# Kernel tuning notes

Hardware: AMD Instinct MI355X
Metric: run time of the kernel (lower is better)

## Reference

```python
import jax, jax.numpy as jnp
import numpy as np


def setup_inputs() -> dict:
    key = jax.random.key(0)
    k1, k2, k3 = jax.random.split(key, 3)
    m, n, d = 4096, 8192, 128
    sub_graph = jax.random.uniform(k1, (m, n), dtype=jnp.float32)
    sub_x = jax.random.normal(k2, (m, d), dtype=jnp.float32)
    all_x = jax.random.normal(k3, (n, d), dtype=jnp.float32)
    return {"sub_graph": sub_graph, "sub_x": sub_x, "all_x": all_x}


def reference(sub_graph, sub_x, all_x):
    # graph_loss, 2D branch. Algebraically identical to the torch code:
    #   trace(X^T diag(d) X) = sum_i d_i * ||x_i||^2
    #   trace(A^T G B)       = sum(A * (G @ B))
    # This avoids materializing the [m,m]/[n,n] diag matrices.
    row_deg = sub_graph.sum(axis=1)            # [m]
    col_deg = sub_graph.sum(axis=0)            # [n]
    term0 = jnp.sum(row_deg * jnp.sum(sub_x * sub_x, axis=1))
    term1 = jnp.sum(col_deg * jnp.sum(all_x * all_x, axis=1))
    cross = jnp.sum(sub_x * (sub_graph @ all_x))
    loss = term0 + term1 - 2.0 * cross
    m, n = sub_graph.shape
    return loss / (m * n)
```

## Files before the change

### kernel.cpp

```cpp
#include <hip/hip_runtime.h>
#include <hip/hip_bf16.h>

#define M 4096
#define N 8192
#define D 128

typedef __attribute__((ext_vector_type(8))) short short8_t;
typedef __attribute__((ext_vector_type(16))) float f32x16;

__device__ inline unsigned short f2bf(float f) {
    union { float f; unsigned u; } v; v.f = f;
    unsigned r = v.u + 0x7FFFu + ((v.u >> 16) & 1u);
    return (unsigned short)(r >> 16);
}


__global__ __launch_bounds__(256) void prep_kernel(const float* __restrict__ sub_x,
                                                   const float* __restrict__ all_x,
                                                   float* __restrict__ ws,
                                                   float* __restrict__ out) {
    const int wave = threadIdx.x >> 6;
    const int lane = threadIdx.x & 63;
    const int row  = blockIdx.x * 4 + wave;

    unsigned* sxb = (unsigned*)(ws + M + N);
    unsigned* axb = sxb + (size_t)M * 64;

    const float* src; float* ndst; unsigned* tdst; int r, R;
    if (row < M) { r = row;     src = sub_x + (size_t)r * D; ndst = ws + r;     tdst = sxb; R = M; }
    else         { r = row - M; src = all_x + (size_t)r * D; ndst = ws + M + r; tdst = axb; R = N; }

    const float2 v = ((const float2*)src)[lane];

    float s = v.x * v.x + v.y * v.y;
    #pragma unroll
    for (int off = 32; off > 0; off >>= 1) s += __shfl_down(s, off, 64);
    if (lane == 0) ndst[0] = s;

    const unsigned p = ((unsigned)f2bf(v.y) << 16) | (unsigned)f2bf(v.x);
    const int k8 = lane >> 2, q = lane & 3;
    tdst[((size_t)k8 * R + r) * 4 + q] = p;

    if (blockIdx.x == 0 && threadIdx.x == 0) out[0] = 0.0f;
}

__global__ __launch_bounds__(256, 3) void graph_loss_kernel(const float* __restrict__ G,
                                                            const float* __restrict__ ws,
                                                            float* __restrict__ out) {
    __shared__ float red[4];

    const int tid  = threadIdx.x;
    const int lane = tid & 63;
    const int w    = tid >> 6;
    const int c    = lane & 31;
    const int hw   = lane >> 5;

    const int ti = blockIdx.x >> 6;
    const int tj = blockIdx.x & 63;
    const int i0 = ti * 128;
    const int j0 = tj * 128;

    const float* sxn = ws;
    const float* axn = ws + M;
    const uint4* sxb = (const uint4*)(ws + M + N);
    const uint4* axb = sxb + (size_t)16 * M;

    const float* gbase = G + (size_t)(i0 + w * 32 + 4 * hw) * N + j0 + c;

    float gv[2][16];
    #pragma unroll
    for (int r = 0; r < 16; ++r)
        gv[0][r] = gbase[(size_t)((r & 3) + 8 * (r >> 2)) * N];

    short8_t a_frag[8];
    #pragma unroll
    for (int kk = 0; kk < 8; ++kk) {
        const uint4 t = sxb[(size_t)(kk * 2 + hw) * M + i0 + w * 32 + c];
        a_frag[kk] = *(const short8_t*)&t;
    }

    float sxv[16];
    #pragma unroll
    for (int r = 0; r < 16; ++r)
        sxv[r] = sxn[i0 + w * 32 + (r & 3) + 8 * (r >> 2) + 4 * hw];

    float axv[4];
    #pragma unroll
    for (int jt = 0; jt < 4; ++jt)
        axv[jt] = axn[j0 + jt * 32 + c];

    const uint4* bbase = axb + (size_t)hw * N + j0 + c;

    float local = 0.0f;

    #pragma unroll
    for (int jt = 0; jt < 4; ++jt) {
        if (jt < 3) {
            #pragma unroll
            for (int r = 0; r < 16; ++r)
                gv[(jt + 1) & 1][r] = gbase[(size_t)((r & 3) + 8 * (r >> 2)) * N + (jt + 1) * 32];
        }

        short8_t b[8];
        #pragma unroll
        for (int kk = 0; kk < 8; ++kk) {
            const uint4 t = bbase[(size_t)(kk * 2) * N + jt * 32];
            b[kk] = *(const short8_t*)&t;
        }

        f32x16 acc;
        #pragma unroll
        for (int r = 0; r < 16; ++r) acc[r] = 0.0f;

        #pragma unroll
        for (int kk = 0; kk < 8; ++kk)
            acc = __builtin_amdgcn_mfma_f32_32x32x16_bf16(a_frag[kk], b[kk], acc, 0, 0, 0);

        const float av = axv[jt];
        #pragma unroll
        for (int r = 0; r < 16; ++r)
            local += gv[jt & 1][r] * (sxv[r] + av - 2.0f * acc[r]);
    }

    #pragma unroll
    for (int off = 32; off > 0; off >>= 1) local += __shfl_down(local, off, 64);
    if (lane == 0) red[w] = local;
    __syncthreads();
    if (tid == 0) {
        const float bsum = red[0] + red[1] + red[2] + red[3];
        atomicAdd(out, bsum * (1.0f / 33554432.0f));
    }
}

extern "C" void kernel_launch(void* const* d_in, const int* in_sizes, int n_in,
                              void* d_out, int out_size, void* d_ws, size_t ws_size,
                              hipStream_t stream) {
    const float* G      = (const float*)d_in[0];
    const float* sub_x  = (const float*)d_in[1];
    const float* all_x  = (const float*)d_in[2];
    float* out = (float*)d_out;
    float* ws  = (float*)d_ws;

    prep_kernel<<<(M + N) / 4, 256, 0, stream>>>(sub_x, all_x, ws, out);
    graph_loss_kernel<<<(M / 128) * (N / 128), 256, 0, stream>>>(G, ws, out);
}
```

Measured before the change: 200.2 us.

## Retile to 32x1024 strips with LDS-staged MFMA results and float4 G loads

Changes the block tile from 128x128 to 32 rows by 1024 columns. Each wave computes the 32x32 MFMA tile for its own column chunk and writes the combined weights (row norm + column norm - 2*dot) into a double-buffered LDS array. G is then read as coalesced float4 rows and multiplied against those weights from LDS. The goal is wide, streaming reads of G with software prefetch two chunks ahead, and reuse of the a-fragment across 1024 columns. The cost is a barrier per chunk and extra LDS traffic.

```diff
diff --git a/kernel.cpp b/kernel.cpp
--- a/kernel.cpp
+++ b/kernel.cpp
@@ -4,6 +4,11 @@
 #define M 4096
 #define N 8192
 #define D 128
+
+#define I_T 32
+#define J_T 1024
+#define JC  128
+#define NC  (J_T / JC)
 
 typedef __attribute__((ext_vector_type(8))) short short8_t;
 typedef __attribute__((ext_vector_type(16))) float f32x16;
@@ -13,7 +18,6 @@
     unsigned r = v.u + 0x7FFFu + ((v.u >> 16) & 1u);
     return (unsigned short)(r >> 16);
 }
-
 
 __global__ __launch_bounds__(256) void prep_kernel(const float* __restrict__ sub_x,
                                                    const float* __restrict__ all_x,
@@ -44,9 +48,47 @@
     if (blockIdx.x == 0 && threadIdx.x == 0) out[0] = 0.0f;
 }
 
+#define PHASE(T, GC, PBASE, QBASE)                                                     \
+  {                                                                                    \
+    if ((T) + 1 < NC) {                                                                \
+      _Pragma("unroll")                                                                \
+      for (int kk = 0; kk < 8; ++kk) {                                                 \
+        const uint4 tb = axb[(size_t)(kk * 2 + hw) * N + j0 + ((T) + 1) * JC + w * 32 + c]; \
+        b[kk] = *(const short8_t*)&tb;                                                 \
+      }                                                                                \
+    }                                                                                  \
+    _Pragma("unroll")                                                                  \
+    for (int s = 0; s < 4; ++s) {                                                      \
+      const int rh = 2 * s + hw;                                                       \
+      const int waddr = (PBASE) + (c >> 3) * 1024 + ((rh & 3) + 4 * w) * 64            \
+                        + ((rh >> 2) & 1) * 32 + 4 * (c & 7);                          \
+      const float4 wv = *(const float4*)&wls[waddr];                                   \
+      local += GC[s].x * wv.x + GC[s].y * wv.y + GC[s].z * wv.z + GC[s].w * wv.w;      \
+    }                                                                                  \
+    if ((T) + 2 < NC) {                                                                \
+      _Pragma("unroll")                                                                \
+      for (int s = 0; s < 4; ++s)                                                      \
+        GC[s] = *(const float4*)(gl + (size_t)(2 * s) * N + ((T) + 2) * JC);           \
+    }                                                                                  \
+    if ((T) + 1 < NC) {                                                                \
+      _Pragma("unroll")                                                                \
+      for (int r = 0; r < 16; ++r) acc[r] = 0.0f;                                      \
+      _Pragma("unroll")                                                                \
+      for (int kk = 0; kk < 8; ++kk)                                                   \
+        acc = __builtin_amdgcn_mfma_f32_32x32x16_bf16(a_frag[kk], b[kk], acc, 0, 0, 0);\
+      const float axv = axn[j0 + ((T) + 1) * JC + w * 32 + c];                         \
+      _Pragma("unroll")                                                                \
+      for (int r = 0; r < 16; ++r)                                                     \
+        wls[(QBASE) + w * 1024 + r * 64 + hw * 32 + c] = sxv[r] + axv - 2.0f * acc[r]; \
+      asm volatile("s_waitcnt lgkmcnt(0)" ::: "memory");                               \
+      __builtin_amdgcn_s_barrier();                                                    \
+    }                                                                                  \
+  }
+
 __global__ __launch_bounds__(256, 3) void graph_loss_kernel(const float* __restrict__ G,
                                                             const float* __restrict__ ws,
                                                             float* __restrict__ out) {
+    __shared__ float wls[2 * 4096];
     __shared__ float red[4];
 
     const int tid  = threadIdx.x;
@@ -55,72 +97,70 @@
     const int c    = lane & 31;
     const int hw   = lane >> 5;
 
-    const int ti = blockIdx.x >> 6;
-    const int tj = blockIdx.x & 63;
-    const int i0 = ti * 128;
-    const int j0 = tj * 128;
+    const int ti = blockIdx.x >> 3;
+    const int tj = blockIdx.x & 7;
+    const int i0 = ti * I_T;
+    const int j0 = tj * J_T;
 
     const float* sxn = ws;
     const float* axn = ws + M;
     const uint4* sxb = (const uint4*)(ws + M + N);
     const uint4* axb = sxb + (size_t)16 * M;
 
-    const float* gbase = G + (size_t)(i0 + w * 32 + 4 * hw) * N + j0 + c;
-
-    float gv[2][16];
-    #pragma unroll
-    for (int r = 0; r < 16; ++r)
-        gv[0][r] = gbase[(size_t)((r & 3) + 8 * (r >> 2)) * N];
-
     short8_t a_frag[8];
     #pragma unroll
     for (int kk = 0; kk < 8; ++kk) {
-        const uint4 t = sxb[(size_t)(kk * 2 + hw) * M + i0 + w * 32 + c];
+        const uint4 t = sxb[(size_t)(kk * 2 + hw) * M + i0 + c];
         a_frag[kk] = *(const short8_t*)&t;
     }
-
     float sxv[16];
     #pragma unroll
     for (int r = 0; r < 16; ++r)
-        sxv[r] = sxn[i0 + w * 32 + (r & 3) + 8 * (r >> 2) + 4 * hw];
+        sxv[r] = sxn[i0 + (r & 3) + 8 * (r >> 2) + 4 * hw];
 
-    float axv[4];
-    #pragma unroll
-    for (int jt = 0; jt < 4; ++jt)
-        axv[jt] = axn[j0 + jt * 32 + c];
+    const float* gl = G + (size_t)(i0 + w * 8 + hw) * N + j0 + 4 * c;
 
-    const uint4* bbase = axb + (size_t)hw * N + j0 + c;
-
-    float local = 0.0f;
+    float  local = 0.0f;
+    float4 gA[4], gB[4];
+    f32x16 acc;
+    short8_t b[8];
 
     #pragma unroll
-    for (int jt = 0; jt < 4; ++jt) {
-        if (jt < 3) {
-            #pragma unroll
-            for (int r = 0; r < 16; ++r)
-                gv[(jt + 1) & 1][r] = gbase[(size_t)((r & 3) + 8 * (r >> 2)) * N + (jt + 1) * 32];
-        }
+    for (int kk = 0; kk < 8; ++kk) {
+        const uint4 tb = axb[(size_t)(kk * 2 + hw) * N + j0 + w * 32 + c];
+        b[kk] = *(const short8_t*)&tb;
+    }
+    #pragma unroll
+    for (int s = 0; s < 4; ++s)
+        gA[s] = *(const float4*)(gl + (size_t)(2 * s) * N);
 
-        short8_t b[8];
-        #pragma unroll
-        for (int kk = 0; kk < 8; ++kk) {
-            const uint4 t = bbase[(size_t)(kk * 2) * N + jt * 32];
-            b[kk] = *(const short8_t*)&t;
-        }
+    #pragma unroll
+    for (int r = 0; r < 16; ++r) acc[r] = 0.0f;
+    #pragma unroll
+    for (int kk = 0; kk < 8; ++kk)
+        acc = __builtin_amdgcn_mfma_f32_32x32x16_bf16(a_frag[kk], b[kk], acc, 0, 0, 0);
 
-        f32x16 acc;
-        #pragma unroll
-        for (int r = 0; r < 16; ++r) acc[r] = 0.0f;
+    #pragma unroll
+    for (int s = 0; s < 4; ++s)
+        gB[s] = *(const float4*)(gl + (size_t)(2 * s) * N + JC);
 
-        #pragma unroll
-        for (int kk = 0; kk < 8; ++kk)
-            acc = __builtin_amdgcn_mfma_f32_32x32x16_bf16(a_frag[kk], b[kk], acc, 0, 0, 0);
-
-        const float av = axv[jt];
+    {
+        const float axv = axn[j0 + w * 32 + c];
         #pragma unroll
         for (int r = 0; r < 16; ++r)
-            local += gv[jt & 1][r] * (sxv[r] + av - 2.0f * acc[r]);
+            wls[w * 1024 + r * 64 + hw * 32 + c] = sxv[r] + axv - 2.0f * acc[r];
     }
+    asm volatile("s_waitcnt lgkmcnt(0)" ::: "memory");
+    __builtin_amdgcn_s_barrier();
+
+    PHASE(0, gA, 0, 4096)
+    PHASE(1, gB, 4096, 0)
+    PHASE(2, gA, 0, 4096)
+    PHASE(3, gB, 4096, 0)
+    PHASE(4, gA, 0, 4096)
+    PHASE(5, gB, 4096, 0)
+    PHASE(6, gA, 0, 4096)
+    PHASE(7, gB, 4096, 0)
 
     #pragma unroll
     for (int off = 32; off > 0; off >>= 1) local += __shfl_down(local, off, 64);
@@ -142,5 +182,5 @@
     float* ws  = (float*)d_ws;
 
     prep_kernel<<<(M + N) / 4, 256, 0, stream>>>(sub_x, all_x, ws, out);
-    graph_loss_kernel<<<(M / 128) * (N / 128), 256, 0, stream>>>(G, ws, out);
+    graph_loss_kernel<<<(M / I_T) * (N / J_T), 256, 0, stream>>>(G, ws, out);
 }
```

After: 199.2 us. No clear change (-0.5%).

## Hand-schedule G and B loads with inline asm and partial vmcnt waits

Applied to the files above, without the earlier changes.

Replaces the compiler-generated global loads of the graph tile and bf16 all_x fragments with inline-asm loads that use SGPR base plus VGPR offsets. Explicit s_waitcnt vmcnt(16) lets the next column tile's 16 G loads stay in flight while the current tile's MFMAs and reduction run. The goal is to hide memory latency the compiler was serializing. The risk is that the compiler cannot see the asm loads when it counts its own waits, and the opaque asm blocks may limit scheduling.

```diff
diff --git a/kernel.cpp b/kernel.cpp
--- a/kernel.cpp
+++ b/kernel.cpp
@@ -13,7 +13,6 @@
     unsigned r = v.u + 0x7FFFu + ((v.u >> 16) & 1u);
     return (unsigned short)(r >> 16);
 }
-
 
 __global__ __launch_bounds__(256) void prep_kernel(const float* __restrict__ sub_x,
                                                    const float* __restrict__ all_x,
@@ -44,6 +43,66 @@
     if (blockIdx.x == 0 && threadIdx.x == 0) out[0] = 0.0f;
 }
 
+
+#define GLOAD(dst, vb, DELTA, sb)                                          \
+  { unsigned _t;                                                           \
+    asm volatile("v_add_u32 %1, %3, %2\n\t"                                \
+                 "global_load_dword %0, %1, %4"                            \
+                 : "=v"(dst), "=&v"(_t)                                    \
+                 : "v"(vb), "i"(DELTA), "s"(sb)); }
+
+#define BLOAD(dst, vb, DELTA, sb)                                          \
+  { unsigned _t;                                                           \
+    asm volatile("v_add_u32 %1, %3, %2\n\t"                                \
+                 "global_load_dwordx4 %0, %1, %4"                          \
+                 : "=v"(dst), "=&v"(_t)                                    \
+                 : "v"(vb), "i"(DELTA), "s"(sb)); }
+
+#define B8(JT)                                                             \
+  BLOAD(b[0], vbB, 0 * N * 32 + (JT) * 512, axp)                           \
+  BLOAD(b[1], vbB, 1 * N * 32 + (JT) * 512, axp)                           \
+  BLOAD(b[2], vbB, 2 * N * 32 + (JT) * 512, axp)                           \
+  BLOAD(b[3], vbB, 3 * N * 32 + (JT) * 512, axp)                           \
+  BLOAD(b[4], vbB, 4 * N * 32 + (JT) * 512, axp)                           \
+  BLOAD(b[5], vbB, 5 * N * 32 + (JT) * 512, axp)                           \
+  BLOAD(b[6], vbB, 6 * N * 32 + (JT) * 512, axp)                           \
+  BLOAD(b[7], vbB, 7 * N * 32 + (JT) * 512, axp)
+
+#define G1(GV, R, JN)                                                      \
+  GLOAD(GV[R], vbG, ((((R) & 3) + 8 * ((R) >> 2)) * N * 4 + (JN) * 128), Gp)
+#define G16(GV, JN)                                                        \
+  G1(GV, 0, JN)  G1(GV, 1, JN)  G1(GV, 2, JN)  G1(GV, 3, JN)               \
+  G1(GV, 4, JN)  G1(GV, 5, JN)  G1(GV, 6, JN)  G1(GV, 7, JN)               \
+  G1(GV, 8, JN)  G1(GV, 9, JN)  G1(GV, 10, JN) G1(GV, 11, JN)              \
+  G1(GV, 12, JN) G1(GV, 13, JN) G1(GV, 14, JN) G1(GV, 15, JN)
+
+#define WAITP(NSTR, GV)                                                    \
+  asm volatile("s_waitcnt vmcnt(" NSTR ")"                                 \
+    : "+v"(b[0]), "+v"(b[1]), "+v"(b[2]), "+v"(b[3]),                      \
+      "+v"(b[4]), "+v"(b[5]), "+v"(b[6]), "+v"(b[7]),                      \
+      "+v"(GV[0]),  "+v"(GV[1]),  "+v"(GV[2]),  "+v"(GV[3]),               \
+      "+v"(GV[4]),  "+v"(GV[5]),  "+v"(GV[6]),  "+v"(GV[7]),               \
+      "+v"(GV[8]),  "+v"(GV[9]),  "+v"(GV[10]), "+v"(GV[11]),              \
+      "+v"(GV[12]), "+v"(GV[13]), "+v"(GV[14]), "+v"(GV[15]));
+
+#define PHASE_TAIL(JT, GVC)                                                \
+    f32x16 acc;                                                            \
+    _Pragma("unroll")                                                      \
+    for (int r = 0; r < 16; ++r) acc[r] = 0.0f;                            \
+    _Pragma("unroll")                                                      \
+    for (int kk = 0; kk < 8; ++kk)                                         \
+      acc = __builtin_amdgcn_mfma_f32_32x32x16_bf16(a_frag[kk], b[kk], acc, 0, 0, 0); \
+    const float av = axv[JT];                                              \
+    _Pragma("unroll")                                                      \
+    for (int r = 0; r < 16; ++r)                                           \
+      local += GVC[r] * (sxv[r] + av - 2.0f * acc[r]);
+
+#define PHASE(JT, GVC, GVN)                                                \
+  { B8(JT) G16(GVN, (JT) + 1) WAITP("16", GVC) PHASE_TAIL(JT, GVC) }
+
+#define PHASEL(JT, GVC)                                                    \
+  { B8(JT) WAITP("0", GVC) PHASE_TAIL(JT, GVC) }
+
 __global__ __launch_bounds__(256, 3) void graph_loss_kernel(const float* __restrict__ G,
                                                             const float* __restrict__ ws,
                                                             float* __restrict__ out) {
@@ -65,62 +124,38 @@
     const uint4* sxb = (const uint4*)(ws + M + N);
     const uint4* axb = sxb + (size_t)16 * M;
 
-    const float* gbase = G + (size_t)(i0 + w * 32 + 4 * hw) * N + j0 + c;
-
-    float gv[2][16];
-    #pragma unroll
-    for (int r = 0; r < 16; ++r)
-        gv[0][r] = gbase[(size_t)((r & 3) + 8 * (r >> 2)) * N];
-
     short8_t a_frag[8];
     #pragma unroll
     for (int kk = 0; kk < 8; ++kk) {
         const uint4 t = sxb[(size_t)(kk * 2 + hw) * M + i0 + w * 32 + c];
         a_frag[kk] = *(const short8_t*)&t;
     }
-
     float sxv[16];
     #pragma unroll
     for (int r = 0; r < 16; ++r)
         sxv[r] = sxn[i0 + w * 32 + (r & 3) + 8 * (r >> 2) + 4 * hw];
-
     float axv[4];
     #pragma unroll
     for (int jt = 0; jt < 4; ++jt)
         axv[jt] = axn[j0 + jt * 32 + c];
 
-    const uint4* bbase = axb + (size_t)hw * N + j0 + c;
+    asm volatile("" ::: "memory");
 
+    const unsigned long long Gp  = (unsigned long long)G;
+    const unsigned long long axp = (unsigned long long)axb;
+    const unsigned vbG = (unsigned)((((size_t)(i0 + w * 32 + 4 * hw)) * N + j0 + c) * 4);
+    const unsigned vbB = (unsigned)(((size_t)hw * N + j0 + c) * 16);
+
+    short8_t b[8];
+    float gA[16], gB[16];
     float local = 0.0f;
 
-    #pragma unroll
-    for (int jt = 0; jt < 4; ++jt) {
-        if (jt < 3) {
-            #pragma unroll
-            for (int r = 0; r < 16; ++r)
-                gv[(jt + 1) & 1][r] = gbase[(size_t)((r & 3) + 8 * (r >> 2)) * N + (jt + 1) * 32];
-        }
+    G16(gA, 0)
 
-        short8_t b[8];
-        #pragma unroll
-        for (int kk = 0; kk < 8; ++kk) {
-            const uint4 t = bbase[(size_t)(kk * 2) * N + jt * 32];
-            b[kk] = *(const short8_t*)&t;
-        }
-
-        f32x16 acc;
-        #pragma unroll
-        for (int r = 0; r < 16; ++r) acc[r] = 0.0f;
-
-        #pragma unroll
-        for (int kk = 0; kk < 8; ++kk)
-            acc = __builtin_amdgcn_mfma_f32_32x32x16_bf16(a_frag[kk], b[kk], acc, 0, 0, 0);
-
-        const float av = axv[jt];
-        #pragma unroll
-        for (int r = 0; r < 16; ++r)
-            local += gv[jt & 1][r] * (sxv[r] + av - 2.0f * acc[r]);
-    }
+    PHASE(0, gA, gB)
+    PHASE(1, gB, gA)
+    PHASE(2, gA, gB)
+    PHASEL(3, gB)
 
     #pragma unroll
     for (int off = 32; off > 0; off >>= 1) local += __shfl_down(local, off, 64);
```

New measurement: 204.2 us. 2.0% more time.
